# Performance work log

Measured on AMD Instinct MI355X. Metric: run time of the kernel, lower is better.

The kernel has to match this reference:

```python
import jax, jax.numpy as jnp
import numpy as np

DIMS = [2048, 2048, 2048, 2048, 1000]
BATCH = 1024
N_RELAX = 25
RELAX_LR = 0.3
N_LAYERS = len(DIMS) - 1  # 4 weight matrices, states indexed 0..4


def setup_inputs() -> dict:
    key = jax.random.key(0)
    ks = jax.random.split(key, N_LAYERS + 1)
    inp = {"x": jax.random.normal(ks[0], (BATCH, DIMS[0]), jnp.float32)}
    for i in range(N_LAYERS):
        scale = np.float32(np.sqrt(2.0 / DIMS[i]))
        inp[f"W{i}"] = jax.random.normal(ks[i + 1], (DIMS[i], DIMS[i + 1]), jnp.float32) * scale
    # biases[0] is never used in forward; biases[1..4] init to zeros as in torch code
    for l in range(1, N_LAYERS + 1):
        inp[f"b{l}"] = jnp.zeros((DIMS[l],), jnp.float32)
    return inp


def _rho(t):
    return jnp.clip(t, 0.0, 1.0)


def _relax(x, Ws, bs):
    # bs[l-1] corresponds to original biases[l] (state l's bias), l = 1..N_LAYERS
    # feedforward initialization pass
    states = [x]
    h = x
    for l in range(N_LAYERS):
        h = _rho(h @ Ws[l] + bs[l])
        states.append(h)

    # Gauss-Seidel sweep: states[l-1] already updated this iteration when l uses it
    def sweep(carry, _):
        full = [x] + list(carry)
        for l in range(1, N_LAYERS + 1):
            ds = -full[l] + bs[l - 1] + _rho(full[l - 1]) @ Ws[l - 1]
            if l < N_LAYERS:
                ds = ds + _rho(full[l + 1]) @ Ws[l].T
            full[l] = _rho(full[l] + RELAX_LR * ds)
        return tuple(full[1:]), None

    carry, _ = jax.lax.scan(sweep, tuple(states[1:]), None, length=N_RELAX)
    return carry


def reference(x, W0, W1, W2, W3, b1, b2, b3, b4):
    Ws = [W0, W1, W2, W3]
    bs = [b1, b2, b3, b4]
    states = _relax(x, Ws, bs)
    return states[-1]  # [BATCH, DIMS[-1]]
```

## Files before the change

kernel.cpp:

```cpp
#include <hip/hip_runtime.h>
#include <hip/hip_bf16.h>

typedef _Float16 fp16_t;
typedef _Float16 v8h __attribute__((ext_vector_type(8)));
typedef _Float16 v4h __attribute__((ext_vector_type(4)));
typedef float    v4f __attribute__((ext_vector_type(4)));

#define RELAX_LR 0.3f

__device__ __forceinline__ void async_cp16(const void* g, void* l) {
    __builtin_amdgcn_global_load_lds(
        (const __attribute__((address_space(1))) void*)g,
        (__attribute__((address_space(3))) void*)l, 16, 0, 0);
}

__global__ __launch_bounds__(256, 2) void gemm_splitk_kernel(
    const fp16_t* __restrict__ A1, const fp16_t* __restrict__ B1t, int K1,
    const fp16_t* __restrict__ A2, const fp16_t* __restrict__ B2t, int K2s,
    int CK, fp16_t* __restrict__ part, int Ntot)
{
    __shared__ __align__(16) fp16_t As[2][2][128][32];
    __shared__ __align__(16) fp16_t Bs[2][2][128][32];

    const int tid  = threadIdx.x;
    const int lane = tid & 63;
    const int w    = tid >> 6;
    const int wm   = w >> 1;
    const int wn   = w & 1;
    const int quad = lane >> 4;
    const int lrow = lane & 15;
    const int bm = blockIdx.y, bn = blockIdx.x, z = blockIdx.z;

    int koff = z * CK;
    const fp16_t* A; const fp16_t* Bt; int stride;
    if (koff < K1) { A = A1; Bt = B1t; stride = K1; }
    else           { A = A2; Bt = B2t; stride = K2s; koff -= K1; }

    const int sr = lane >> 2;
    const int sc = (lane & 3) * 8;
    const fp16_t* ag = A  + (size_t)(bm * 128 + 32 * w + sr) * stride + koff + sc;
    const fp16_t* bg = Bt + (size_t)(bn * 128 + 32 * w + sr) * stride + koff + sc;
    const size_t st16 = (size_t)16 * stride;

    v4f acc[4][4] = {};

    const int iters = CK >> 6;

    auto stage = [&](int buf, int kb) {
        const fp16_t* a0 = ag + kb;
        const fp16_t* b0 = bg + kb;
        async_cp16(a0,             &As[buf][0][32 * w     ][0]);
        async_cp16(a0 + st16,      &As[buf][0][32 * w + 16][0]);
        async_cp16(a0 + 32,        &As[buf][1][32 * w     ][0]);
        async_cp16(a0 + 32 + st16, &As[buf][1][32 * w + 16][0]);
        async_cp16(b0,             &Bs[buf][0][32 * w     ][0]);
        async_cp16(b0 + st16,      &Bs[buf][0][32 * w + 16][0]);
        async_cp16(b0 + 32,        &Bs[buf][1][32 * w     ][0]);
        async_cp16(b0 + 32 + st16, &Bs[buf][1][32 * w + 16][0]);
    };

    stage(0, 0);

    for (int it = 0; it < iters; ++it) {
        __syncthreads();
        if (it + 1 < iters) stage((it + 1) & 1, (it + 1) * 64);
        const int cur = it & 1;
        #pragma unroll
        for (int h = 0; h < 2; ++h) {
            v8h af[4], bv[4];
            #pragma unroll
            for (int fm = 0; fm < 4; ++fm)
                af[fm] = *(const v8h*)&As[cur][h][wm * 64 + fm * 16 + lrow][quad * 8];
            #pragma unroll
            for (int fn = 0; fn < 4; ++fn)
                bv[fn] = *(const v8h*)&Bs[cur][h][wn * 64 + fn * 16 + lrow][quad * 8];
            #pragma unroll
            for (int fm = 0; fm < 4; ++fm)
                #pragma unroll
                for (int fn = 0; fn < 4; ++fn)
                    acc[fm][fn] = __builtin_amdgcn_mfma_f32_16x16x32_f16(
                        af[fm], bv[fn], acc[fm][fn], 0, 0, 0);
        }
    }

    fp16_t* po = part + (size_t)z * 1024 * Ntot;
    const int rowbase = bm * 128 + wm * 64 + quad * 4;
    const int colbase = bn * 128 + wn * 64;
    #pragma unroll
    for (int fn = 0; fn < 4; ++fn) {
        const int col = colbase + fn * 16 + lrow;
        #pragma unroll
        for (int fm = 0; fm < 4; ++fm) {
            const int row = rowbase + fm * 16;
            #pragma unroll
            for (int r = 0; r < 4; ++r)
                po[(size_t)(row + r) * Ntot + col] = (fp16_t)acc[fm][fn][r];
        }
    }
}

__global__ __launch_bounds__(256) void reduce_update_kernel(
    const fp16_t* __restrict__ part, int nz,
    const float* __restrict__ bias, const float* __restrict__ s_old,
    float* __restrict__ outf, fp16_t* __restrict__ outb,
    int Ntot, int do_update, int total8)
{
    const int i = blockIdx.x * 256 + threadIdx.x;
    if (i >= total8) return;
    const size_t e = (size_t)i * 8;

    float v[8];
    {
        const v8h p0 = *(const v8h*)(part + e);
        #pragma unroll
        for (int j = 0; j < 8; ++j) v[j] = (float)p0[j];
    }
    for (int z = 1; z < nz; ++z) {
        const v8h p = *(const v8h*)(part + (size_t)z * 1024 * Ntot + e);
        #pragma unroll
        for (int j = 0; j < 8; ++j) v[j] += (float)p[j];
    }
    const int col = (int)e & (Ntot - 1);
    const float4 b0 = *(const float4*)(bias + col);
    const float4 b1 = *(const float4*)(bias + col + 4);
    v[0] += b0.x; v[1] += b0.y; v[2] += b0.z; v[3] += b0.w;
    v[4] += b1.x; v[5] += b1.y; v[6] += b1.z; v[7] += b1.w;
    if (do_update) {
        const float4 s0 = *(const float4*)(s_old + e);
        const float4 s1 = *(const float4*)(s_old + e + 4);
        const float so[8] = {s0.x, s0.y, s0.z, s0.w, s1.x, s1.y, s1.z, s1.w};
        #pragma unroll
        for (int j = 0; j < 8; ++j) v[j] = so[j] + RELAX_LR * (v[j] - so[j]);
    }
    float4 o0, o1;
    #pragma unroll
    for (int j = 0; j < 8; ++j) v[j] = fminf(fmaxf(v[j], 0.f), 1.f);
    o0.x = v[0]; o0.y = v[1]; o0.z = v[2]; o0.w = v[3];
    o1.x = v[4]; o1.y = v[5]; o1.z = v[6]; o1.w = v[7];
    *(float4*)(outf + e)     = o0;
    *(float4*)(outf + e + 4) = o1;
    v8h h;
    #pragma unroll
    for (int j = 0; j < 8; ++j) h[j] = (fp16_t)v[j];
    *(v8h*)(outb + e) = h;
}

__global__ void conv_w_kernel(const float* __restrict__ W, int R, int C,
                              fp16_t* Wb, fp16_t* __restrict__ WbT,
                              int Rp, int Cp)
{
    __shared__ float t[32][33];
    const int tx = threadIdx.x & 31;
    const int ty = threadIdx.x >> 5;
    const int r0 = blockIdx.y * 32;
    const int c0 = blockIdx.x * 32;
    #pragma unroll
    for (int i = 0; i < 4; ++i) {
        const int r = r0 + ty + i * 8;
        const int c = c0 + tx;
        float v = 0.f;
        if (r < R && c < C) v = W[(size_t)r * C + c];
        t[ty + i * 8][tx] = v;
    }
    __syncthreads();
    if (Wb) {
        #pragma unroll
        for (int i = 0; i < 4; ++i) {
            const int r = r0 + ty + i * 8;
            const int c = c0 + tx;
            if (r < Rp && c < Cp) Wb[(size_t)r * Cp + c] = (fp16_t)t[ty + i * 8][tx];
        }
    }
    #pragma unroll
    for (int i = 0; i < 4; ++i) {
        const int cc = c0 + ty + i * 8;
        const int rr = r0 + tx;
        if (cc < Cp && rr < Rp) WbT[(size_t)cc * Rp + rr] = (fp16_t)t[tx][ty + i * 8];
    }
}

__global__ void conv_x_kernel(const float* __restrict__ x,
                              fp16_t* __restrict__ xb, fp16_t* __restrict__ rxb, int n)
{
    const int i = blockIdx.x * blockDim.x + threadIdx.x;
    if (i < n) {
        const float v = x[i];
        xb[i]  = (fp16_t)v;
        rxb[i] = (fp16_t)fminf(fmaxf(v, 0.f), 1.f);
    }
}

__global__ void pad_b4_kernel(const float* __restrict__ b4, float* __restrict__ b4p)
{
    const int i = blockIdx.x * blockDim.x + threadIdx.x;
    if (i < 1024) b4p[i] = (i < 1000) ? b4[i] : 0.f;
}

__global__ void out_copy_kernel(const float* __restrict__ s4f, float* __restrict__ out)
{
    const int i = blockIdx.x * blockDim.x + threadIdx.x;
    if (i < 1024 * 1000) {
        const int row = i / 1000;
        const int col = i - row * 1000;
        out[i] = s4f[(size_t)row * 1024 + col];
    }
}

extern "C" void kernel_launch(void* const* d_in, const int* in_sizes, int n_in,
                              void* d_out, int out_size, void* d_ws, size_t ws_size,
                              hipStream_t stream)
{
    const float* x  = (const float*)d_in[0];
    const float* W0 = (const float*)d_in[1];
    const float* W1 = (const float*)d_in[2];
    const float* W2 = (const float*)d_in[3];
    const float* W3 = (const float*)d_in[4];
    const float* b1 = (const float*)d_in[5];
    const float* b2 = (const float*)d_in[6];
    const float* b3 = (const float*)d_in[7];
    const float* b4 = (const float*)d_in[8];
    float* out = (float*)d_out;

    char* p = (char*)d_ws;
    auto alloc = [&](size_t bytes) {
        char* q = p;
        p += (bytes + 255) & ~(size_t)255;
        return q;
    };

    fp16_t* xb   = (fp16_t*)alloc((size_t)1024 * 2048 * 2);
    fp16_t* rxb  = (fp16_t*)alloc((size_t)1024 * 2048 * 2);
    fp16_t* Wb1  = (fp16_t*)alloc((size_t)2048 * 2048 * 2);
    fp16_t* Wb2  = (fp16_t*)alloc((size_t)2048 * 2048 * 2);
    fp16_t* Wb3  = (fp16_t*)alloc((size_t)2048 * 1024 * 2);
    fp16_t* WbT0 = (fp16_t*)alloc((size_t)2048 * 2048 * 2);
    fp16_t* WbT1 = (fp16_t*)alloc((size_t)2048 * 2048 * 2);
    fp16_t* WbT2 = (fp16_t*)alloc((size_t)2048 * 2048 * 2);
    fp16_t* WbT3 = (fp16_t*)alloc((size_t)1024 * 2048 * 2);
    float*  s1f  = (float*)alloc((size_t)1024 * 2048 * 4);
    float*  s2f  = (float*)alloc((size_t)1024 * 2048 * 4);
    float*  s3f  = (float*)alloc((size_t)1024 * 2048 * 4);
    float*  s4f  = (float*)alloc((size_t)1024 * 1024 * 4);
    fp16_t* s1b  = (fp16_t*)alloc((size_t)1024 * 2048 * 2);
    fp16_t* s2b  = (fp16_t*)alloc((size_t)1024 * 2048 * 2);
    fp16_t* s3b  = (fp16_t*)alloc((size_t)1024 * 2048 * 2);
    fp16_t* s4b  = (fp16_t*)alloc((size_t)1024 * 1024 * 2);
    float*  b4p  = (float*)alloc(1024 * 4);
    fp16_t* part = (fp16_t*)alloc((size_t)4 * 1024 * 2048 * 2);
    (void)ws_size; (void)in_sizes; (void)n_in; (void)out_size;

    conv_x_kernel<<<(1024 * 2048 + 255) / 256, 256, 0, stream>>>(x, xb, rxb, 1024 * 2048);
    pad_b4_kernel<<<4, 256, 0, stream>>>(b4, b4p);
    conv_w_kernel<<<dim3(64, 64), 256, 0, stream>>>(W0, 2048, 2048, nullptr, WbT0, 2048, 2048);
    conv_w_kernel<<<dim3(64, 64), 256, 0, stream>>>(W1, 2048, 2048, Wb1, WbT1, 2048, 2048);
    conv_w_kernel<<<dim3(64, 64), 256, 0, stream>>>(W2, 2048, 2048, Wb2, WbT2, 2048, 2048);
    conv_w_kernel<<<dim3(32, 64), 256, 0, stream>>>(W3, 2048, 1000, Wb3, WbT3, 2048, 1024);

    const dim3 blk(256);
    const int t8_2048 = 1024 * 2048 / 8;
    const int t8_1024 = 1024 * 1024 / 8;
    const int rg2048 = t8_2048 / 256;
    const int rg1024 = t8_1024 / 256;

    gemm_splitk_kernel<<<dim3(16, 8, 4), blk, 0, stream>>>(xb,  WbT0, 2048, nullptr, nullptr, 0, 512, part, 2048);
    reduce_update_kernel<<<rg2048, blk, 0, stream>>>(part, 4, b1, nullptr, s1f, s1b, 2048, 0, t8_2048);
    gemm_splitk_kernel<<<dim3(16, 8, 4), blk, 0, stream>>>(s1b, WbT1, 2048, nullptr, nullptr, 0, 512, part, 2048);
    reduce_update_kernel<<<rg2048, blk, 0, stream>>>(part, 4, b2, nullptr, s2f, s2b, 2048, 0, t8_2048);
    gemm_splitk_kernel<<<dim3(16, 8, 4), blk, 0, stream>>>(s2b, WbT2, 2048, nullptr, nullptr, 0, 512, part, 2048);
    reduce_update_kernel<<<rg2048, blk, 0, stream>>>(part, 4, b3, nullptr, s3f, s3b, 2048, 0, t8_2048);
    gemm_splitk_kernel<<<dim3(8, 8, 8), blk, 0, stream>>>(s3b, WbT3, 2048, nullptr, nullptr, 0, 256, part, 1024);
    reduce_update_kernel<<<rg1024, blk, 0, stream>>>(part, 8, b4p, nullptr, s4f, s4b, 1024, 0, t8_1024);

    for (int it = 0; it < 25; ++it) {
        gemm_splitk_kernel<<<dim3(16, 8, 4), blk, 0, stream>>>(rxb, WbT0, 2048, s2b, Wb1, 2048, 1024, part, 2048);
        reduce_update_kernel<<<rg2048, blk, 0, stream>>>(part, 4, b1, s1f, s1f, s1b, 2048, 1, t8_2048);
        gemm_splitk_kernel<<<dim3(16, 8, 4), blk, 0, stream>>>(s1b, WbT1, 2048, s3b, Wb2, 2048, 1024, part, 2048);
        reduce_update_kernel<<<rg2048, blk, 0, stream>>>(part, 4, b2, s2f, s2f, s2b, 2048, 1, t8_2048);
        gemm_splitk_kernel<<<dim3(16, 8, 3), blk, 0, stream>>>(s2b, WbT2, 2048, s4b, Wb3, 1024, 1024, part, 2048);
        reduce_update_kernel<<<rg2048, blk, 0, stream>>>(part, 3, b3, s3f, s3f, s3b, 2048, 1, t8_2048);
        gemm_splitk_kernel<<<dim3(8, 8, 8), blk, 0, stream>>>(s3b, WbT3, 2048, nullptr, nullptr, 0, 256, part, 1024);
        reduce_update_kernel<<<rg1024, blk, 0, stream>>>(part, 8, b4p, s4f, s4f, s4b, 1024, 1, t8_1024);
    }

    out_copy_kernel<<<(1024 * 1000 + 255) / 256, 256, 0, stream>>>(s4f, out);
}
```

Before: 2.955 ms.

## Drop fp32 state copies, keep fp16 states, and remap split-K grid for balance

Removes the fp32 state buffers so the reduce/update kernel reads and writes only fp16 states, cutting global memory traffic per update. The GEMM now uses a flat 512-block grid with a custom block-to-tile mapping meant to improve scheduling and L2 locality. Layer 3 now splits as 2+2 instead of 2+1 (per-split K 512), so all 512 blocks carry more even work. Keeping the relaxation state only in fp16 accumulates rounding error over 25 iterations and the output is produced from fp16.

```diff
diff --git a/kernel.cpp b/kernel.cpp
--- a/kernel.cpp
+++ b/kernel.cpp
@@ -3,7 +3,6 @@
 
 typedef _Float16 fp16_t;
 typedef _Float16 v8h __attribute__((ext_vector_type(8)));
-typedef _Float16 v4h __attribute__((ext_vector_type(4)));
 typedef float    v4f __attribute__((ext_vector_type(4)));
 
 #define RELAX_LR 0.3f
@@ -15,9 +14,9 @@
 }
 
 __global__ __launch_bounds__(256, 2) void gemm_splitk_kernel(
-    const fp16_t* __restrict__ A1, const fp16_t* __restrict__ B1t, int K1,
-    const fp16_t* __restrict__ A2, const fp16_t* __restrict__ B2t, int K2s,
-    int CK, fp16_t* __restrict__ part, int Ntot)
+    const fp16_t* __restrict__ A1, const fp16_t* __restrict__ B1t, int K1, int CK1, int nz1,
+    const fp16_t* __restrict__ A2, const fp16_t* __restrict__ B2t, int K2s, int CK2,
+    fp16_t* __restrict__ part, int Ntot)
 {
     __shared__ __align__(16) fp16_t As[2][2][128][32];
     __shared__ __align__(16) fp16_t Bs[2][2][128][32];
@@ -29,12 +28,19 @@
     const int wn   = w & 1;
     const int quad = lane >> 4;
     const int lrow = lane & 15;
-    const int bm = blockIdx.y, bn = blockIdx.x, z = blockIdx.z;
-
-    int koff = z * CK;
-    const fp16_t* A; const fp16_t* Bt; int stride;
-    if (koff < K1) { A = A1; Bt = B1t; stride = K1; }
-    else           { A = A2; Bt = B2t; stride = K2s; koff -= K1; }
+
+    const int blk  = blockIdx.x;
+    const int low3 = blk & 7;
+    const int g    = blk >> 3;
+    const int bm   = g & 7;
+    const int c    = (g >> 3) * 8 + low3;
+    int bn, z;
+    if (Ntot == 2048) { bn = c >> 2; z = c & 3; }
+    else              { bn = c >> 3; z = c & 7; }
+
+    const fp16_t *A, *Bt; int stride, koff, CK;
+    if (z < nz1) { A = A1; Bt = B1t; stride = K1;  CK = CK1; koff = z * CK1; }
+    else         { A = A2; Bt = B2t; stride = K2s; CK = CK2; koff = (z - nz1) * CK2; }
 
     const int sr = lane >> 2;
     const int sc = (lane & 3) * 8;
@@ -43,7 +49,6 @@
     const size_t st16 = (size_t)16 * stride;
 
     v4f acc[4][4] = {};
-
     const int iters = CK >> 6;
 
     auto stage = [&](int buf, int kb) {
@@ -101,9 +106,8 @@
 
 __global__ __launch_bounds__(256) void reduce_update_kernel(
     const fp16_t* __restrict__ part, int nz,
-    const float* __restrict__ bias, const float* __restrict__ s_old,
-    float* __restrict__ outf, fp16_t* __restrict__ outb,
-    int Ntot, int do_update, int total8)
+    const float* __restrict__ bias, const fp16_t* s_old,
+    fp16_t* outb, int Ntot, int do_update, int total8)
 {
     const int i = blockIdx.x * 256 + threadIdx.x;
     if (i >= total8) return;
@@ -126,22 +130,16 @@
     v[0] += b0.x; v[1] += b0.y; v[2] += b0.z; v[3] += b0.w;
     v[4] += b1.x; v[5] += b1.y; v[6] += b1.z; v[7] += b1.w;
     if (do_update) {
-        const float4 s0 = *(const float4*)(s_old + e);
-        const float4 s1 = *(const float4*)(s_old + e + 4);
-        const float so[8] = {s0.x, s0.y, s0.z, s0.w, s1.x, s1.y, s1.z, s1.w};
-        #pragma unroll
-        for (int j = 0; j < 8; ++j) v[j] = so[j] + RELAX_LR * (v[j] - so[j]);
-    }
-    float4 o0, o1;
-    #pragma unroll
-    for (int j = 0; j < 8; ++j) v[j] = fminf(fmaxf(v[j], 0.f), 1.f);
-    o0.x = v[0]; o0.y = v[1]; o0.z = v[2]; o0.w = v[3];
-    o1.x = v[4]; o1.y = v[5]; o1.z = v[6]; o1.w = v[7];
-    *(float4*)(outf + e)     = o0;
-    *(float4*)(outf + e + 4) = o1;
+        const v8h so = *(const v8h*)(s_old + e);
+        #pragma unroll
+        for (int j = 0; j < 8; ++j) {
+            const float s = (float)so[j];
+            v[j] = s + RELAX_LR * (v[j] - s);
+        }
+    }
     v8h h;
     #pragma unroll
-    for (int j = 0; j < 8; ++j) h[j] = (fp16_t)v[j];
+    for (int j = 0; j < 8; ++j) h[j] = (fp16_t)fminf(fmaxf(v[j], 0.f), 1.f);
     *(v8h*)(outb + e) = h;
 }
 
@@ -196,13 +194,13 @@
     if (i < 1024) b4p[i] = (i < 1000) ? b4[i] : 0.f;
 }
 
-__global__ void out_copy_kernel(const float* __restrict__ s4f, float* __restrict__ out)
+__global__ void out_copy_kernel(const fp16_t* __restrict__ s4b, float* __restrict__ out)
 {
     const int i = blockIdx.x * blockDim.x + threadIdx.x;
     if (i < 1024 * 1000) {
         const int row = i / 1000;
         const int col = i - row * 1000;
-        out[i] = s4f[(size_t)row * 1024 + col];
+        out[i] = (float)s4b[(size_t)row * 1024 + col];
     }
 }
 
@@ -237,10 +235,6 @@
     fp16_t* WbT1 = (fp16_t*)alloc((size_t)2048 * 2048 * 2);
     fp16_t* WbT2 = (fp16_t*)alloc((size_t)2048 * 2048 * 2);
     fp16_t* WbT3 = (fp16_t*)alloc((size_t)1024 * 2048 * 2);
-    float*  s1f  = (float*)alloc((size_t)1024 * 2048 * 4);
-    float*  s2f  = (float*)alloc((size_t)1024 * 2048 * 4);
-    float*  s3f  = (float*)alloc((size_t)1024 * 2048 * 4);
-    float*  s4f  = (float*)alloc((size_t)1024 * 1024 * 4);
     fp16_t* s1b  = (fp16_t*)alloc((size_t)1024 * 2048 * 2);
     fp16_t* s2b  = (fp16_t*)alloc((size_t)1024 * 2048 * 2);
     fp16_t* s3b  = (fp16_t*)alloc((size_t)1024 * 2048 * 2);
@@ -257,30 +251,31 @@
     conv_w_kernel<<<dim3(32, 64), 256, 0, stream>>>(W3, 2048, 1000, Wb3, WbT3, 2048, 1024);
 
     const dim3 blk(256);
+    const dim3 g512(512);
     const int t8_2048 = 1024 * 2048 / 8;
     const int t8_1024 = 1024 * 1024 / 8;
     const int rg2048 = t8_2048 / 256;
     const int rg1024 = t8_1024 / 256;
 
-    gemm_splitk_kernel<<<dim3(16, 8, 4), blk, 0, stream>>>(xb,  WbT0, 2048, nullptr, nullptr, 0, 512, part, 2048);
-    reduce_update_kernel<<<rg2048, blk, 0, stream>>>(part, 4, b1, nullptr, s1f, s1b, 2048, 0, t8_2048);
-    gemm_splitk_kernel<<<dim3(16, 8, 4), blk, 0, stream>>>(s1b, WbT1, 2048, nullptr, nullptr, 0, 512, part, 2048);
-    reduce_update_kernel<<<rg2048, blk, 0, stream>>>(part, 4, b2, nullptr, s2f, s2b, 2048, 0, t8_2048);
-    gemm_splitk_kernel<<<dim3(16, 8, 4), blk, 0, stream>>>(s2b, WbT2, 2048, nullptr, nullptr, 0, 512, part, 2048);
-    reduce_update_kernel<<<rg2048, blk, 0, stream>>>(part, 4, b3, nullptr, s3f, s3b, 2048, 0, t8_2048);
-    gemm_splitk_kernel<<<dim3(8, 8, 8), blk, 0, stream>>>(s3b, WbT3, 2048, nullptr, nullptr, 0, 256, part, 1024);
-    reduce_update_kernel<<<rg1024, blk, 0, stream>>>(part, 8, b4p, nullptr, s4f, s4b, 1024, 0, t8_1024);
+    gemm_splitk_kernel<<<g512, blk, 0, stream>>>(xb,  WbT0, 2048, 512, 4, nullptr, nullptr, 0, 0, part, 2048);
+    reduce_update_kernel<<<rg2048, blk, 0, stream>>>(part, 4, b1, nullptr, s1b, 2048, 0, t8_2048);
+    gemm_splitk_kernel<<<g512, blk, 0, stream>>>(s1b, WbT1, 2048, 512, 4, nullptr, nullptr, 0, 0, part, 2048);
+    reduce_update_kernel<<<rg2048, blk, 0, stream>>>(part, 4, b2, nullptr, s2b, 2048, 0, t8_2048);
+    gemm_splitk_kernel<<<g512, blk, 0, stream>>>(s2b, WbT2, 2048, 512, 4, nullptr, nullptr, 0, 0, part, 2048);
+    reduce_update_kernel<<<rg2048, blk, 0, stream>>>(part, 4, b3, nullptr, s3b, 2048, 0, t8_2048);
+    gemm_splitk_kernel<<<g512, blk, 0, stream>>>(s3b, WbT3, 2048, 256, 8, nullptr, nullptr, 0, 0, part, 1024);
+    reduce_update_kernel<<<rg1024, blk, 0, stream>>>(part, 8, b4p, nullptr, s4b, 1024, 0, t8_1024);
 
     for (int it = 0; it < 25; ++it) {
-        gemm_splitk_kernel<<<dim3(16, 8, 4), blk, 0, stream>>>(rxb, WbT0, 2048, s2b, Wb1, 2048, 1024, part, 2048);
-        reduce_update_kernel<<<rg2048, blk, 0, stream>>>(part, 4, b1, s1f, s1f, s1b, 2048, 1, t8_2048);
-        gemm_splitk_kernel<<<dim3(16, 8, 4), blk, 0, stream>>>(s1b, WbT1, 2048, s3b, Wb2, 2048, 1024, part, 2048);
-        reduce_update_kernel<<<rg2048, blk, 0, stream>>>(part, 4, b2, s2f, s2f, s2b, 2048, 1, t8_2048);
-        gemm_splitk_kernel<<<dim3(16, 8, 3), blk, 0, stream>>>(s2b, WbT2, 2048, s4b, Wb3, 1024, 1024, part, 2048);
-        reduce_update_kernel<<<rg2048, blk, 0, stream>>>(part, 3, b3, s3f, s3f, s3b, 2048, 1, t8_2048);
-        gemm_splitk_kernel<<<dim3(8, 8, 8), blk, 0, stream>>>(s3b, WbT3, 2048, nullptr, nullptr, 0, 256, part, 1024);
-        reduce_update_kernel<<<rg1024, blk, 0, stream>>>(part, 8, b4p, s4f, s4f, s4b, 1024, 1, t8_1024);
-    }
-
-    out_copy_kernel<<<(1024 * 1000 + 255) / 256, 256, 0, stream>>>(s4f, out);
-}
+        gemm_splitk_kernel<<<g512, blk, 0, stream>>>(rxb, WbT0, 2048, 1024, 2, s2b, Wb1, 2048, 1024, part, 2048);
+        reduce_update_kernel<<<rg2048, blk, 0, stream>>>(part, 4, b1, s1b, s1b, 2048, 1, t8_2048);
+        gemm_splitk_kernel<<<g512, blk, 0, stream>>>(s1b, WbT1, 2048, 1024, 2, s3b, Wb2, 2048, 1024, part, 2048);
+        reduce_update_kernel<<<rg2048, blk, 0, stream>>>(part, 4, b2, s2b, s2b, 2048, 1, t8_2048);
+        gemm_splitk_kernel<<<g512, blk, 0, stream>>>(s2b, WbT2, 2048, 1024, 2, s4b, Wb3, 1024, 512, part, 2048);
+        reduce_update_kernel<<<rg2048, blk, 0, stream>>>(part, 4, b3, s3b, s3b, 2048, 1, t8_2048);
+        gemm_splitk_kernel<<<g512, blk, 0, stream>>>(s3b, WbT3, 2048, 256, 8, nullptr, nullptr, 0, 0, part, 1024);
+        reduce_update_kernel<<<rg1024, blk, 0, stream>>>(part, 8, b4p, s4b, s4b, 1024, 1, t8_1024);
+    }
+
+    out_copy_kernel<<<(1024 * 1000 + 255) / 256, 256, 0, stream>>>(s4b, out);
+}
```

New measurement: 2.853 ms. 3.4% less time.
